# Kernel optimization log

Hardware: AMD Instinct MI355X
Metric: run time of the kernel (lower is better)

Reference implementation:

```python
import jax, jax.numpy as jnp
import numpy as np

B, S, D = 1, 2048, 2048
H, KVH = 32, 8
HD = D // H          # 64
N_REP = H // KVH     # 4
ROPE_THETA = 10000.0
NEG = -1e9


def setup_inputs() -> dict:
    key = jax.random.key(0)
    ks = jax.random.split(key, 8)
    x = jax.random.normal(ks[0], (B, S, D), dtype=jnp.float32)
    # RoPE tables: freqs_cis[t, j] = exp(i * t * theta^{-2j/HD}), j in [0, HD/2)
    inv_freq = 1.0 / (ROPE_THETA ** (jnp.arange(0, HD, 2, dtype=jnp.float32) / HD))
    angles = jnp.arange(S, dtype=jnp.float32)[:, None] * inv_freq[None, :]  # (S, HD/2)
    freqs_cos = jnp.cos(angles)
    freqs_sin = jnp.sin(angles)
    # causal additive mask (S, S)
    mask = jnp.where(jnp.tril(jnp.ones((S, S), dtype=bool)), 0.0, NEG).astype(jnp.float32)
    sc = 0.02
    wq = jax.random.normal(ks[1], (D, H * HD), dtype=jnp.float32) * sc
    wk = jax.random.normal(ks[2], (D, KVH * HD), dtype=jnp.float32) * sc
    wv = jax.random.normal(ks[3], (D, KVH * HD), dtype=jnp.float32) * sc
    wo = jax.random.normal(ks[4], (H * HD, D), dtype=jnp.float32) * sc
    fw = jax.random.normal(ks[5], (HD, HD), dtype=jnp.float32) * sc
    fb = jnp.zeros((HD,), dtype=jnp.float32)
    return {"x": x, "freqs_cos": freqs_cos, "freqs_sin": freqs_sin, "mask": mask,
            "wq": wq, "wk": wk, "wv": wv, "wo": wo, "fw": fw, "fb": fb,
            "start_pos": 0}


def _rope(t, cos, sin):
    # t: (B, S, h, HD) -> complex rotate pairs along last dim
    tr = t.reshape(*t.shape[:-1], HD // 2, 2)
    c = cos[None, :, None, :]  # (1, S, 1, HD/2)
    s = sin[None, :, None, :]
    re = tr[..., 0] * c - tr[..., 1] * s
    im = tr[..., 0] * s + tr[..., 1] * c
    return jnp.stack([re, im], axis=-1).reshape(t.shape)


def reference(x, freqs_cos, freqs_sin, mask, wq, wk, wv, wo, fw, fb, start_pos):
    b, s, _ = x.shape
    xq = (x @ wq).reshape(b, s, H, HD)
    xk = (x @ wk).reshape(b, s, KVH, HD)
    xv = (x @ wv).reshape(b, s, KVH, HD)
    xq = _rope(xq, freqs_cos, freqs_sin)
    xk = _rope(xk, freqs_cos, freqs_sin)
    # GQA: repeat kv heads (repeat_interleave on head dim)
    keys = jnp.repeat(xk, N_REP, axis=2)    # (b, s, H, HD)
    values = jnp.repeat(xv, N_REP, axis=2)
    q = xq.transpose(0, 2, 1, 3)            # (b, H, s, HD)
    k = keys.transpose(0, 2, 1, 3)
    v = values.transpose(0, 2, 1, 3)
    scores = jnp.einsum("bhqd,bhkd->bhqk", q, k) / np.sqrt(HD).astype(np.float32)
    scores = scores + mask[None, None, :, :]
    probs = jax.nn.softmax(scores.astype(jnp.float32), axis=-1).astype(q.dtype)
    out = jnp.einsum("bhqk,bhkd->bhqd", probs, v)  # (b, H, s, HD)
    # shared per-head FFN: Linear(HD, HD) + SiLU, vectorized over heads
    out = jax.nn.silu(out @ fw + fb)
    out = out.transpose(0, 2, 1, 3).reshape(b, s, H * HD)
    return out @ wo
```

## Files before the change

### kernel.cpp

```cpp
#include <hip/hip_runtime.h>
#include <stdint.h>

#define S_LEN 2048
#define DMODEL 2048
#define NH 32
#define NKV 8
#define HD 64

typedef __attribute__((ext_vector_type(8))) __bf16 bf16x8;
typedef __attribute__((ext_vector_type(4))) float f32x4;

__device__ __forceinline__ unsigned short f2bf(float f) {
    union { float f; uint32_t u; } v; v.f = f;
    uint32_t u = v.u;
    u += 0x7FFFu + ((u >> 16) & 1u);
    return (unsigned short)(u >> 16);
}

__device__ __forceinline__ uint32_t cvt_pk_bf16(float lo, float hi) {
    uint32_t r;
    asm("v_cvt_pk_bf16_f32 %0, %1, %2" : "=v"(r) : "v"(lo), "v"(hi));
    return r;
}

#define GLDS16(g, l)                                                          \
    __builtin_amdgcn_global_load_lds(                                         \
        (const __attribute__((address_space(1))) unsigned int*)(g),           \
        (__attribute__((address_space(3))) unsigned int*)(l), 16, 0, 0)

__global__ void cast_bf16_kernel(const float* __restrict__ src,
                                 unsigned short* __restrict__ dst, int n) {
    int g = (blockIdx.x * blockDim.x + threadIdx.x) * 8;
    if (g >= n) return;
    float4 a = *(const float4*)&src[g];
    float4 b = *(const float4*)&src[g + 4];
    unsigned short o[8];
    o[0] = f2bf(a.x); o[1] = f2bf(a.y); o[2] = f2bf(a.z); o[3] = f2bf(a.w);
    o[4] = f2bf(b.x); o[5] = f2bf(b.y); o[6] = f2bf(b.z); o[7] = f2bf(b.w);
    *(uint4*)&dst[g] = *(const uint4*)o;
}

__global__ void transpose_cast_kernel(const float* __restrict__ src,
                                      unsigned short* __restrict__ dst,
                                      int R, int C) {
    __shared__ float tile[32][33];
    int c0 = blockIdx.x * 32, r0 = blockIdx.y * 32;
    int tx = threadIdx.x, ty = threadIdx.y;
#pragma unroll
    for (int i = 0; i < 32; i += 8)
        tile[ty + i][tx] = src[(size_t)(r0 + ty + i) * C + c0 + tx];
    __syncthreads();
#pragma unroll
    for (int i = 0; i < 32; i += 8)
        dst[(size_t)(c0 + ty + i) * R + r0 + tx] = f2bf(tile[tx][ty + i]);
}

__global__ __launch_bounds__(256) void gemm_bt_kernel(
    const unsigned short* __restrict__ A, const unsigned short* __restrict__ BT,
    float* __restrict__ C0, float* __restrict__ C1, int M, int N,
    int Kstride, int Klen) {
    __shared__ unsigned short As[2][128 * 32];
    __shared__ unsigned short Bs[2][128 * 32];
    const int t = threadIdx.x;
    const int lane = t & 63, wave = t >> 6;
    const int wr = wave >> 1, wc = wave & 1;
    const int m0 = blockIdx.x * 128, n0 = blockIdx.y * 128;
    const int koff = blockIdx.z * Klen;
    float* __restrict__ C = blockIdx.z ? C1 : C0;
    const int l15 = lane & 15, lhi = lane >> 4;
    f32x4 acc[4][4] = {};
    const unsigned short* ga = A + (size_t)(m0 + (t >> 2)) * Kstride + koff + (t & 3) * 8;
    const unsigned short* gb = BT + (size_t)(n0 + (t >> 2)) * Kstride + koff + (t & 3) * 8;

    GLDS16(ga, &As[0][t * 8]);
    GLDS16(ga + (size_t)64 * Kstride, &As[0][t * 8 + 64 * 32]);
    GLDS16(gb, &Bs[0][t * 8]);
    GLDS16(gb + (size_t)64 * Kstride, &Bs[0][t * 8 + 64 * 32]);
    __syncthreads();

    int cur = 0;
    for (int k0 = 0; k0 < Klen; k0 += 32) {
        if (k0 + 32 < Klen) {
            GLDS16(ga + k0 + 32, &As[cur ^ 1][t * 8]);
            GLDS16(ga + (size_t)64 * Kstride + k0 + 32, &As[cur ^ 1][t * 8 + 64 * 32]);
            GLDS16(gb + k0 + 32, &Bs[cur ^ 1][t * 8]);
            GLDS16(gb + (size_t)64 * Kstride + k0 + 32, &Bs[cur ^ 1][t * 8 + 64 * 32]);
        }
        bf16x8 af[4], bfr[4];
#pragma unroll
        for (int m = 0; m < 4; m++)
            af[m] = *(const bf16x8*)&As[cur][(wr * 64 + m * 16 + l15) * 32 + lhi * 8];
#pragma unroll
        for (int n = 0; n < 4; n++)
            bfr[n] = *(const bf16x8*)&Bs[cur][(wc * 64 + n * 16 + l15) * 32 + lhi * 8];
#pragma unroll
        for (int m = 0; m < 4; m++)
#pragma unroll
            for (int n = 0; n < 4; n++)
                acc[m][n] = __builtin_amdgcn_mfma_f32_16x16x32_bf16(
                    af[m], bfr[n], acc[m][n], 0, 0, 0);
        __syncthreads();
        cur ^= 1;
    }
#pragma unroll
    for (int m = 0; m < 4; m++) {
        int row = m0 + wr * 64 + m * 16 + lhi * 4;
#pragma unroll
        for (int n = 0; n < 4; n++) {
            int col = n0 + wc * 64 + n * 16 + l15;
#pragma unroll
            for (int r = 0; r < 4; r++)
                C[(size_t)(row + r) * N + col] = acc[m][n][r];
        }
    }
}

__global__ void add_f32_kernel(float* __restrict__ out,
                               const float* __restrict__ p1, int n4) {
    int g = blockIdx.x * blockDim.x + threadIdx.x;
    if (g >= n4) return;
    float4 a = *(const float4*)&out[g * 4];
    float4 b = *(const float4*)&p1[g * 4];
    a.x += b.x; a.y += b.y; a.z += b.z; a.w += b.w;
    *(float4*)&out[g * 4] = a;
}

__global__ void rope_q_kernel(const float* __restrict__ Cqkv,
                              const float* __restrict__ cb,
                              const float* __restrict__ sb,
                              unsigned short* __restrict__ Q) {
    const float CS = 0.125f * 1.44269504f;
    int g = blockIdx.x * 256 + threadIdx.x;
    int i = g & 31;
    int h = (g >> 5) & 31;
    int s = g >> 10;
    float2 v = *(const float2*)&Cqkv[(size_t)s * 3072 + h * 64 + 2 * i];
    float cc = cb[s * 32 + i], ss = sb[s * 32 + i];
    ushort2 o;
    o.x = f2bf((v.x * cc - v.y * ss) * CS);
    o.y = f2bf((v.x * ss + v.y * cc) * CS);
    *(ushort2*)&Q[(size_t)h * (S_LEN * HD) + s * HD + 2 * i] = o;
}

__global__ void rope_k_kernel(const float* __restrict__ Cqkv,
                              const float* __restrict__ cb,
                              const float* __restrict__ sb,
                              unsigned short* __restrict__ Kb) {
    int g = blockIdx.x * 256 + threadIdx.x;
    int i = g & 31;
    int kvh = (g >> 5) & 7;
    int s = g >> 8;
    float2 v = *(const float2*)&Cqkv[(size_t)s * 3072 + 2048 + kvh * 64 + 2 * i];
    float cc = cb[s * 32 + i], ss = sb[s * 32 + i];
    ushort2 o;
    o.x = f2bf(v.x * cc - v.y * ss);
    o.y = f2bf(v.x * ss + v.y * cc);
    *(ushort2*)&Kb[(size_t)kvh * (S_LEN * HD) + s * HD + 2 * i] = o;
}

__global__ void v_transpose_kernel(const float* __restrict__ Cqkv,
                                   unsigned short* __restrict__ VT) {
    __shared__ float tile[32][33];
    int kvh = blockIdx.z;
    int d0 = blockIdx.x * 32, s0 = blockIdx.y * 32;
    int tx = threadIdx.x, ty = threadIdx.y;
#pragma unroll
    for (int i = 0; i < 32; i += 8)
        tile[ty + i][tx] =
            Cqkv[(size_t)(s0 + ty + i) * 3072 + 2560 + kvh * 64 + d0 + tx];
    __syncthreads();
#pragma unroll
    for (int i = 0; i < 32; i += 8)
        VT[(size_t)kvh * (HD * S_LEN) + (size_t)(d0 + ty + i) * S_LEN + s0 + tx] =
            f2bf(tile[tx][ty + i]);
}

__global__ __launch_bounds__(256) void flash_kernel(
    const unsigned short* __restrict__ Q, const unsigned short* __restrict__ Kg,
    const unsigned short* __restrict__ VTg, unsigned short* __restrict__ O) {
    __shared__ unsigned short Ks[2][4096];
    __shared__ unsigned short Vs[2][4096];
    const int t = threadIdx.x, lane = t & 63, wave = t >> 6;
    const int l15 = lane & 15, lhi = lane >> 4;
    const int bid = blockIdx.x;
    const int h = bid & 31;
    const int u = bid >> 5;
    const int grp = u >> 3, pos = u & 7;
    const int qt = (grp & 1) ? (grp * 8 + 7 - pos) : (grp * 8 + pos);
    const int kvh = h >> 2;

    const int srow = t >> 3;
    const int scol = ((t & 7) * 8) ^ ((srow & 7) * 8);
    const unsigned short* gk = Kg + ((size_t)kvh * S_LEN + srow) * HD + scol;
    const unsigned short* gv = VTg + ((size_t)kvh * HD + srow) * S_LEN + scol;

    const int q0 = qt * 64;
    const int nt = qt + 1;
    const int wq = q0 + wave * 16;
    const int q = wq + l15;

    const unsigned short* qp = Q + ((size_t)h * S_LEN + q) * HD + lhi * 8;
    bf16x8 qf0 = *(const bf16x8*)qp;
    bf16x8 qf1 = *(const bf16x8*)(qp + 32);

    f32x4 oacc[4] = {};
    float mrun = -1e30f, lrun = 0.f;

    GLDS16(gk, &Ks[0][t * 8]);
    GLDS16(gk + (size_t)32 * HD, &Ks[0][t * 8 + 2048]);
    GLDS16(gv, &Vs[0][t * 8]);
    GLDS16(gv + (size_t)32 * S_LEN, &Vs[0][t * 8 + 2048]);
    __syncthreads();

    int cur = 0;
#pragma unroll 1
    for (int kt = 0; kt < nt; ++kt) {
        const int kv0 = kt * 64;
        if (kt + 1 < nt) {
            GLDS16(gk + (size_t)(kv0 + 64) * HD, &Ks[cur ^ 1][t * 8]);
            GLDS16(gk + (size_t)(kv0 + 96) * HD, &Ks[cur ^ 1][t * 8 + 2048]);
            GLDS16(gv + (kv0 + 64), &Vs[cur ^ 1][t * 8]);
            GLDS16(gv + (size_t)32 * S_LEN + (kv0 + 64), &Vs[cur ^ 1][t * 8 + 2048]);
        }
        f32x4 sacc[4] = {};
#pragma unroll
        for (int nb = 0; nb < 4; nb++) {
            int krow = nb * 16 + l15;
            const unsigned short* kb = &Ks[cur][krow * 64];
            int sw = (krow & 7) * 8;
            bf16x8 k0v = *(const bf16x8*)&kb[(lhi * 8) ^ sw];
            bf16x8 k1v = *(const bf16x8*)&kb[(32 + lhi * 8) ^ sw];
            sacc[nb] = __builtin_amdgcn_mfma_f32_16x16x32_bf16(k0v, qf0, sacc[nb], 0, 0, 0);
            sacc[nb] = __builtin_amdgcn_mfma_f32_16x16x32_bf16(k1v, qf1, sacc[nb], 0, 0, 0);
        }
        float pv[4][4];
        float lm = -1e30f;
        if (kv0 + 63 <= wq) {
#pragma unroll
            for (int nb = 0; nb < 4; nb++)
#pragma unroll
                for (int r = 0; r < 4; r++) {
                    float sv = sacc[nb][r];
                    pv[nb][r] = sv;
                    lm = fmaxf(lm, sv);
                }
        } else {
#pragma unroll
            for (int nb = 0; nb < 4; nb++) {
                int kvb = kv0 + nb * 16 + lhi * 4;
#pragma unroll
                for (int r = 0; r < 4; r++) {
                    float sv = (kvb + r <= q) ? sacc[nb][r] : -1e30f;
                    pv[nb][r] = sv;
                    lm = fmaxf(lm, sv);
                }
            }
        }
        if (!__all(lm - mrun <= 8.f)) {
            float rm = fmaxf(lm, __shfl_xor(lm, 16));
            rm = fmaxf(rm, __shfl_xor(rm, 32));
            float mnew = fmaxf(mrun, rm);
            float sc = exp2f(mrun - mnew);
            mrun = mnew;
            lrun *= sc;
#pragma unroll
            for (int db = 0; db < 4; db++) oacc[db] *= sc;
        }
        float rs = 0.f;
#pragma unroll
        for (int nb = 0; nb < 4; nb++)
#pragma unroll
            for (int r = 0; r < 4; r++) {
                float e = exp2f(pv[nb][r] - mrun);
                pv[nb][r] = e;
                rs += e;
            }
        lrun += rs;
        uint32_t pka[4], pkb[4];
#pragma unroll
        for (int nb = 0; nb < 4; nb++) {
            pka[nb] = cvt_pk_bf16(pv[nb][0], pv[nb][1]);
            pkb[nb] = cvt_pk_bf16(pv[nb][2], pv[nb][3]);
        }
        const bool selB = ((lhi >> 1) & 1);
        const bool hiR = (lhi & 1);
        const bool sendA = ((lhi ^ (lhi >> 1)) & 1);
#pragma unroll
        for (int ks = 0; ks < 2; ks++) {
            uint32_t A0 = selB ? pka[2 * ks + 1] : pka[2 * ks];
            uint32_t A1 = selB ? pkb[2 * ks + 1] : pkb[2 * ks];
            uint32_t W0 = selB ? pka[2 * ks] : pka[2 * ks + 1];
            uint32_t W1 = selB ? pkb[2 * ks] : pkb[2 * ks + 1];
            uint32_t B0 = __shfl_xor((int)W0, 32);
            uint32_t B1 = __shfl_xor((int)W1, 32);
            uint32_t S0 = sendA ? A0 : B0, S1 = sendA ? A1 : B1;
            uint32_t R0 = __shfl_xor((int)S0, 16);
            uint32_t R1 = __shfl_xor((int)S1, 16);
            uint32_t F0 = hiR ? R0 : (selB ? B0 : A0);
            uint32_t F1 = hiR ? R1 : (selB ? B1 : A1);
            uint32_t F2 = hiR ? (selB ? A0 : B0) : R0;
            uint32_t F3 = hiR ? (selB ? A1 : B1) : R1;
            uint4 fu = {F0, F1, F2, F3};
            bf16x8 pfrag = *(const bf16x8*)&fu;
#pragma unroll
            for (int db = 0; db < 4; db++) {
                int vrow = db * 16 + l15;
                bf16x8 vf = *(const bf16x8*)&Vs[cur][vrow * 64 + ((ks * 32 + lhi * 8) ^ ((vrow & 7) * 8))];
                oacc[db] = __builtin_amdgcn_mfma_f32_16x16x32_bf16(vf, pfrag, oacc[db], 0, 0, 0);
            }
        }
        __syncthreads();
        cur ^= 1;
    }
    lrun += __shfl_xor(lrun, 16);
    lrun += __shfl_xor(lrun, 32);
    float rinv = 1.f / lrun;
#pragma unroll
    for (int db = 0; db < 4; db++) {
        uint32_t o0 = cvt_pk_bf16(oacc[db][0] * rinv, oacc[db][1] * rinv);
        uint32_t o1 = cvt_pk_bf16(oacc[db][2] * rinv, oacc[db][3] * rinv);
        uint2 ov = {o0, o1};
        *(uint2*)&O[((size_t)h * S_LEN + q) * HD + db * 16 + lhi * 4] = ov;
    }
}

__global__ __launch_bounds__(256) void fw_silu_kernel(
    const unsigned short* __restrict__ AT, const unsigned short* __restrict__ fwT,
    const float* __restrict__ fb, unsigned short* __restrict__ h2) {
    const int t = threadIdx.x, lane = t & 63, wave = t >> 6;
    const int l15 = lane & 15, lhi = lane >> 4;
    const int r0 = blockIdx.x * 64 + wave * 16;
    const unsigned short* ap = AT + (size_t)(r0 + l15) * HD + lhi * 8;
    bf16x8 a0 = *(const bf16x8*)ap;
    bf16x8 a1 = *(const bf16x8*)(ap + 32);
    f32x4 acc[4] = {};
#pragma unroll
    for (int nb = 0; nb < 4; nb++) {
        const unsigned short* bp = fwT + (size_t)(nb * 16 + l15) * HD + lhi * 8;
        bf16x8 b0 = *(const bf16x8*)bp;
        bf16x8 b1 = *(const bf16x8*)(bp + 32);
        acc[nb] = __builtin_amdgcn_mfma_f32_16x16x32_bf16(a0, b0, acc[nb], 0, 0, 0);
        acc[nb] = __builtin_amdgcn_mfma_f32_16x16x32_bf16(a1, b1, acc[nb], 0, 0, 0);
    }
#pragma unroll
    for (int nb = 0; nb < 4; nb++) {
        int col = nb * 16 + l15;
        float bias = fb[col];
#pragma unroll
        for (int r = 0; r < 4; r++) {
            int row = r0 + lhi * 4 + r;
            int s = row & (S_LEN - 1), hh = row >> 11;
            float x = acc[nb][r] + bias;
            float sg = 1.f / (1.f + exp2f(-x * 1.44269504f));
            h2[(size_t)s * DMODEL + hh * HD + col] = f2bf(x * sg);
        }
    }
}

extern "C" void kernel_launch(void* const* d_in, const int* in_sizes, int n_in,
                              void* d_out, int out_size, void* d_ws, size_t ws_size,
                              hipStream_t stream) {
    const float* x = (const float*)d_in[0];
    const float* fcos = (const float*)d_in[1];
    const float* fsin = (const float*)d_in[2];
    const float* wq = (const float*)d_in[4];
    const float* wk = (const float*)d_in[5];
    const float* wv = (const float*)d_in[6];
    const float* wo = (const float*)d_in[7];
    const float* fw = (const float*)d_in[8];
    const float* fb = (const float*)d_in[9];
    float* out = (float*)d_out;

    char* ws = (char*)d_ws;
    size_t off = 0;
    auto alloc = [&](size_t bytes) {
        void* p = ws + off;
        off += (bytes + 255) & ~(size_t)255;
        return p;
    };
    unsigned short* wqkvT = (unsigned short*)alloc((size_t)3072 * 2048 * 2);
    unsigned short* woT   = (unsigned short*)alloc((size_t)2048 * 2048 * 2);
    unsigned short* fwT   = (unsigned short*)alloc((size_t)64 * 64 * 2);
    float*          Cqkv  = (float*)alloc((size_t)2048 * 3072 * 4);
    unsigned short* Qb    = (unsigned short*)alloc((size_t)NH * S_LEN * HD * 2);
    unsigned short* Kb    = (unsigned short*)alloc((size_t)NKV * S_LEN * HD * 2);
    unsigned short* VT    = (unsigned short*)alloc((size_t)NKV * HD * S_LEN * 2);
    unsigned short* xb    = (unsigned short*)alloc((size_t)2048 * 2048 * 2);
    unsigned short* attn = (unsigned short*)Cqkv;
    float* P1 = (float*)((char*)Cqkv + (size_t)NH * S_LEN * HD * 2);
    unsigned short* h2 = xb;

    dim3 tb(32, 8);
    cast_bf16_kernel<<<2048, 256, 0, stream>>>(x, xb, 2048 * 2048);
    transpose_cast_kernel<<<dim3(64, 64), tb, 0, stream>>>(wq, wqkvT, 2048, 2048);
    transpose_cast_kernel<<<dim3(16, 64), tb, 0, stream>>>(wk, wqkvT + (size_t)2048 * 2048, 2048, 512);
    transpose_cast_kernel<<<dim3(16, 64), tb, 0, stream>>>(wv, wqkvT + (size_t)2560 * 2048, 2048, 512);
    transpose_cast_kernel<<<dim3(64, 64), tb, 0, stream>>>(wo, woT, 2048, 2048);
    transpose_cast_kernel<<<dim3(2, 2), tb, 0, stream>>>(fw, fwT, 64, 64);

    gemm_bt_kernel<<<dim3(16, 24, 1), 256, 0, stream>>>(xb, wqkvT, Cqkv, nullptr,
                                                        2048, 3072, 2048, 2048);

    rope_q_kernel<<<8192, 256, 0, stream>>>(Cqkv, fcos, fsin, Qb);
    rope_k_kernel<<<2048, 256, 0, stream>>>(Cqkv, fcos, fsin, Kb);
    v_transpose_kernel<<<dim3(2, 64, 8), tb, 0, stream>>>(Cqkv, VT);

    flash_kernel<<<1024, 256, 0, stream>>>(Qb, Kb, VT, attn);

    fw_silu_kernel<<<1024, 256, 0, stream>>>(attn, fwT, fb, h2);

    gemm_bt_kernel<<<dim3(16, 16, 2), 256, 0, stream>>>(h2, woT, out, P1,
                                                        2048, 2048, 2048, 1024);
    add_f32_kernel<<<4096, 256, 0, stream>>>(out, P1, 1048576);
}
```

Baseline: 187.9 us.

## Rework flash attention with 32x32 MFMA, 128-row Q tiles, paired causal work and triple buffering

The flash attention kernel now gives each wave 32 query rows and uses 32x32x16 MFMA instructions, so each block covers 128 queries. Each block handles two paired Q tiles (s and 15-s) to balance causal work, and the grid shrinks to 256 blocks. K/V staging moves to a three-buffer ring with explicit vmcnt waits, so loads run two tiles ahead. The goals are better MFMA efficiency, fewer P shuffles and less load latency. The cost is fewer blocks than CUs (lower occupancy), and waves past the causal limit sit idle.

```diff
diff --git a/kernel.cpp b/kernel.cpp
--- a/kernel.cpp
+++ b/kernel.cpp
@@ -9,6 +9,7 @@
 
 typedef __attribute__((ext_vector_type(8))) __bf16 bf16x8;
 typedef __attribute__((ext_vector_type(4))) float f32x4;
+typedef __attribute__((ext_vector_type(16))) float f32x16;
 
 __device__ __forceinline__ unsigned short f2bf(float f) {
     union { float f; uint32_t u; } v; v.f = f;
@@ -178,15 +179,12 @@
 __global__ __launch_bounds__(256) void flash_kernel(
     const unsigned short* __restrict__ Q, const unsigned short* __restrict__ Kg,
     const unsigned short* __restrict__ VTg, unsigned short* __restrict__ O) {
-    __shared__ unsigned short Ks[2][4096];
-    __shared__ unsigned short Vs[2][4096];
+    __shared__ unsigned short Ks[3][4096];
+    __shared__ unsigned short Vs[3][4096];
     const int t = threadIdx.x, lane = t & 63, wave = t >> 6;
-    const int l15 = lane & 15, lhi = lane >> 4;
+    const int l31 = lane & 31, hi = lane >> 5;
     const int bid = blockIdx.x;
-    const int h = bid & 31;
-    const int u = bid >> 5;
-    const int grp = u >> 3, pos = u & 7;
-    const int qt = (grp & 1) ? (grp * 8 + 7 - pos) : (grp * 8 + pos);
+    const int h = bid & 31, pr = bid >> 5;
     const int kvh = h >> 2;
 
     const int srow = t >> 3;
@@ -194,133 +192,153 @@
     const unsigned short* gk = Kg + ((size_t)kvh * S_LEN + srow) * HD + scol;
     const unsigned short* gv = VTg + ((size_t)kvh * HD + srow) * S_LEN + scol;
 
-    const int q0 = qt * 64;
-    const int nt = qt + 1;
-    const int wq = q0 + wave * 16;
-    const int q = wq + l15;
-
-    const unsigned short* qp = Q + ((size_t)h * S_LEN + q) * HD + lhi * 8;
-    bf16x8 qf0 = *(const bf16x8*)qp;
-    bf16x8 qf1 = *(const bf16x8*)(qp + 32);
-
-    f32x4 oacc[4] = {};
-    float mrun = -1e30f, lrun = 0.f;
-
-    GLDS16(gk, &Ks[0][t * 8]);
-    GLDS16(gk + (size_t)32 * HD, &Ks[0][t * 8 + 2048]);
-    GLDS16(gv, &Vs[0][t * 8]);
-    GLDS16(gv + (size_t)32 * S_LEN, &Vs[0][t * 8 + 2048]);
-    __syncthreads();
-
-    int cur = 0;
 #pragma unroll 1
-    for (int kt = 0; kt < nt; ++kt) {
-        const int kv0 = kt * 64;
-        if (kt + 1 < nt) {
-            GLDS16(gk + (size_t)(kv0 + 64) * HD, &Ks[cur ^ 1][t * 8]);
-            GLDS16(gk + (size_t)(kv0 + 96) * HD, &Ks[cur ^ 1][t * 8 + 2048]);
-            GLDS16(gv + (kv0 + 64), &Vs[cur ^ 1][t * 8]);
-            GLDS16(gv + (size_t)32 * S_LEN + (kv0 + 64), &Vs[cur ^ 1][t * 8 + 2048]);
+    for (int item = 0; item < 2; ++item) {
+        const int s = item ? (15 - pr) : pr;
+        const int q0 = s * 128;
+        const int nt = 2 * s + 2;
+        const int qw0 = q0 + wave * 32;
+        const int q = qw0 + l31;
+
+        const unsigned short* qp = Q + ((size_t)h * S_LEN + q) * HD + hi * 8;
+        bf16x8 qf0 = *(const bf16x8*)(qp);
+        bf16x8 qf1 = *(const bf16x8*)(qp + 16);
+        bf16x8 qf2 = *(const bf16x8*)(qp + 32);
+        bf16x8 qf3 = *(const bf16x8*)(qp + 48);
+
+        f32x16 oacc0 = {}, oacc1 = {};
+        float mrun = -1e30f, lrun = 0.f;
+
+        asm volatile("s_waitcnt vmcnt(0)" ::: "memory");
+        __builtin_amdgcn_s_barrier();
+        GLDS16(gk, &Ks[0][t * 8]);
+        GLDS16(gk + (size_t)32 * HD, &Ks[0][t * 8 + 2048]);
+        GLDS16(gv, &Vs[0][t * 8]);
+        GLDS16(gv + (size_t)32 * S_LEN, &Vs[0][t * 8 + 2048]);
+        GLDS16(gk + (size_t)64 * HD, &Ks[1][t * 8]);
+        GLDS16(gk + (size_t)96 * HD, &Ks[1][t * 8 + 2048]);
+        GLDS16(gv + 64, &Vs[1][t * 8]);
+        GLDS16(gv + (size_t)32 * S_LEN + 64, &Vs[1][t * 8 + 2048]);
+
+#pragma unroll 1
+        for (int kt = 0; kt < nt; ++kt) {
+            if (kt + 1 < nt) asm volatile("s_waitcnt vmcnt(4)" ::: "memory");
+            else             asm volatile("s_waitcnt vmcnt(0)" ::: "memory");
+            __builtin_amdgcn_s_barrier();
+            __builtin_amdgcn_sched_barrier(0);
+            if (kt + 2 < nt) {
+                const int pb = (kt + 2) % 3;
+                const size_t kvp = (size_t)(kt + 2) * 64;
+                GLDS16(gk + kvp * HD, &Ks[pb][t * 8]);
+                GLDS16(gk + (kvp + 32) * HD, &Ks[pb][t * 8 + 2048]);
+                GLDS16(gv + kvp, &Vs[pb][t * 8]);
+                GLDS16(gv + (size_t)32 * S_LEN + kvp, &Vs[pb][t * 8 + 2048]);
+            }
+            const int kv0 = kt * 64;
+            if (kv0 > qw0 + 31) continue;
+            const int cb = kt % 3;
+            const unsigned short* ksb = Ks[cb];
+            const unsigned short* vsb = Vs[cb];
+            const int sw = (l31 & 7) * 8;
+            f32x16 s0 = {}, s1 = {};
+#pragma unroll
+            for (int kc = 0; kc < 4; kc++) {
+                bf16x8 k0 = *(const bf16x8*)&ksb[l31 * 64 + ((16 * kc + 8 * hi) ^ sw)];
+                bf16x8 k1 = *(const bf16x8*)&ksb[(32 + l31) * 64 + ((16 * kc + 8 * hi) ^ sw)];
+                bf16x8 qc = (kc == 0) ? qf0 : (kc == 1) ? qf1 : (kc == 2) ? qf2 : qf3;
+                s0 = __builtin_amdgcn_mfma_f32_32x32x16_bf16(k0, qc, s0, 0, 0, 0);
+                s1 = __builtin_amdgcn_mfma_f32_32x32x16_bf16(k1, qc, s1, 0, 0, 0);
+            }
+            float p0[16], p1[16];
+            if (kv0 + 63 <= qw0) {
+#pragma unroll
+                for (int r = 0; r < 16; r++) { p0[r] = s0[r]; p1[r] = s1[r]; }
+            } else {
+#pragma unroll
+                for (int r = 0; r < 16; r++) {
+                    int rr = (r & 3) + 8 * (r >> 2) + 4 * hi;
+                    p0[r] = (kv0 + rr <= q) ? s0[r] : -1e30f;
+                    p1[r] = (kv0 + 32 + rr <= q) ? s1[r] : -1e30f;
+                }
+            }
+            float t8[8];
+#pragma unroll
+            for (int r = 0; r < 8; r++)
+                t8[r] = fmaxf(fmaxf(p0[r], p0[r + 8]), fmaxf(p1[r], p1[r + 8]));
+            float lm = fmaxf(fmaxf(fmaxf(t8[0], t8[4]), fmaxf(t8[1], t8[5])),
+                             fmaxf(fmaxf(t8[2], t8[6]), fmaxf(t8[3], t8[7])));
+            if (!__all(lm - mrun <= 8.f)) {
+                float rm = fmaxf(lm, __shfl_xor(lm, 32));
+                float mnew = fmaxf(mrun, rm);
+                float sc = exp2f(mrun - mnew);
+                mrun = mnew;
+                lrun *= sc;
+                oacc0 *= sc;
+                oacc1 *= sc;
+            }
+#pragma unroll
+            for (int r = 0; r < 16; r++) {
+                p0[r] = exp2f(p0[r] - mrun);
+                p1[r] = exp2f(p1[r] - mrun);
+            }
+            float sA = 0.f, sB = 0.f, sC = 0.f, sD = 0.f;
+#pragma unroll
+            for (int r = 0; r < 4; r++) {
+                sA += p0[r] + p1[r];
+                sB += p0[r + 4] + p1[r + 4];
+                sC += p0[r + 8] + p1[r + 8];
+                sD += p0[r + 12] + p1[r + 12];
+            }
+            lrun += (sA + sB) + (sC + sD);
+            bf16x8 pf[4];
+#pragma unroll
+            for (int kc = 0; kc < 4; kc++) {
+                const int sub = (kc & 1) * 8;
+                uint32_t Wl0, Wl1, Wh0, Wh1;
+                if (kc < 2) {
+                    Wl0 = cvt_pk_bf16(p0[sub + 0], p0[sub + 1]);
+                    Wl1 = cvt_pk_bf16(p0[sub + 2], p0[sub + 3]);
+                    Wh0 = cvt_pk_bf16(p0[sub + 4], p0[sub + 5]);
+                    Wh1 = cvt_pk_bf16(p0[sub + 6], p0[sub + 7]);
+                } else {
+                    Wl0 = cvt_pk_bf16(p1[sub + 0], p1[sub + 1]);
+                    Wl1 = cvt_pk_bf16(p1[sub + 2], p1[sub + 3]);
+                    Wh0 = cvt_pk_bf16(p1[sub + 4], p1[sub + 5]);
+                    Wh1 = cvt_pk_bf16(p1[sub + 6], p1[sub + 7]);
+                }
+                uint32_t sw0 = hi ? Wl0 : Wh0, sw1 = hi ? Wl1 : Wh1;
+                uint32_t rc0 = __shfl_xor((int)sw0, 32);
+                uint32_t rc1 = __shfl_xor((int)sw1, 32);
+                uint32_t kp0 = hi ? Wh0 : Wl0, kp1 = hi ? Wh1 : Wl1;
+                uint32_t F0 = hi ? rc0 : kp0;
+                uint32_t F1 = hi ? rc1 : kp1;
+                uint32_t F2 = hi ? kp0 : rc0;
+                uint32_t F3 = hi ? kp1 : rc1;
+                uint4 fu = {F0, F1, F2, F3};
+                pf[kc] = *(const bf16x8*)&fu;
+            }
+#pragma unroll
+            for (int kc = 0; kc < 4; kc++) {
+                bf16x8 v0 = *(const bf16x8*)&vsb[l31 * 64 + ((16 * kc + 8 * hi) ^ sw)];
+                bf16x8 v1 = *(const bf16x8*)&vsb[(32 + l31) * 64 + ((16 * kc + 8 * hi) ^ sw)];
+                oacc0 = __builtin_amdgcn_mfma_f32_32x32x16_bf16(v0, pf[kc], oacc0, 0, 0, 0);
+                oacc1 = __builtin_amdgcn_mfma_f32_32x32x16_bf16(v1, pf[kc], oacc1, 0, 0, 0);
+            }
         }
-        f32x4 sacc[4] = {};
-#pragma unroll
-        for (int nb = 0; nb < 4; nb++) {
-            int krow = nb * 16 + l15;
-            const unsigned short* kb = &Ks[cur][krow * 64];
-            int sw = (krow & 7) * 8;
-            bf16x8 k0v = *(const bf16x8*)&kb[(lhi * 8) ^ sw];
-            bf16x8 k1v = *(const bf16x8*)&kb[(32 + lhi * 8) ^ sw];
-            sacc[nb] = __builtin_amdgcn_mfma_f32_16x16x32_bf16(k0v, qf0, sacc[nb], 0, 0, 0);
-            sacc[nb] = __builtin_amdgcn_mfma_f32_16x16x32_bf16(k1v, qf1, sacc[nb], 0, 0, 0);
+        lrun += __shfl_xor(lrun, 32);
+        float rinv = 1.f / lrun;
+        unsigned short* ob = O + ((size_t)h * S_LEN + q) * HD + 4 * hi;
+#pragma unroll
+        for (int g = 0; g < 4; g++) {
+            uint32_t a0 = cvt_pk_bf16(oacc0[4 * g] * rinv, oacc0[4 * g + 1] * rinv);
+            uint32_t a1 = cvt_pk_bf16(oacc0[4 * g + 2] * rinv, oacc0[4 * g + 3] * rinv);
+            uint2 u0 = {a0, a1};
+            *(uint2*)(ob + 8 * g) = u0;
+            uint32_t b0 = cvt_pk_bf16(oacc1[4 * g] * rinv, oacc1[4 * g + 1] * rinv);
+            uint32_t b1 = cvt_pk_bf16(oacc1[4 * g + 2] * rinv, oacc1[4 * g + 3] * rinv);
+            uint2 u1 = {b0, b1};
+            *(uint2*)(ob + 32 + 8 * g) = u1;
         }
-        float pv[4][4];
-        float lm = -1e30f;
-        if (kv0 + 63 <= wq) {
-#pragma unroll
-            for (int nb = 0; nb < 4; nb++)
-#pragma unroll
-                for (int r = 0; r < 4; r++) {
-                    float sv = sacc[nb][r];
-                    pv[nb][r] = sv;
-                    lm = fmaxf(lm, sv);
-                }
-        } else {
-#pragma unroll
-            for (int nb = 0; nb < 4; nb++) {
-                int kvb = kv0 + nb * 16 + lhi * 4;
-#pragma unroll
-                for (int r = 0; r < 4; r++) {
-                    float sv = (kvb + r <= q) ? sacc[nb][r] : -1e30f;
-                    pv[nb][r] = sv;
-                    lm = fmaxf(lm, sv);
-                }
-            }
-        }
-        if (!__all(lm - mrun <= 8.f)) {
-            float rm = fmaxf(lm, __shfl_xor(lm, 16));
-            rm = fmaxf(rm, __shfl_xor(rm, 32));
-            float mnew = fmaxf(mrun, rm);
-            float sc = exp2f(mrun - mnew);
-            mrun = mnew;
-            lrun *= sc;
-#pragma unroll
-            for (int db = 0; db < 4; db++) oacc[db] *= sc;
-        }
-        float rs = 0.f;
-#pragma unroll
-        for (int nb = 0; nb < 4; nb++)
-#pragma unroll
-            for (int r = 0; r < 4; r++) {
-                float e = exp2f(pv[nb][r] - mrun);
-                pv[nb][r] = e;
-                rs += e;
-            }
-        lrun += rs;
-        uint32_t pka[4], pkb[4];
-#pragma unroll
-        for (int nb = 0; nb < 4; nb++) {
-            pka[nb] = cvt_pk_bf16(pv[nb][0], pv[nb][1]);
-            pkb[nb] = cvt_pk_bf16(pv[nb][2], pv[nb][3]);
-        }
-        const bool selB = ((lhi >> 1) & 1);
-        const bool hiR = (lhi & 1);
-        const bool sendA = ((lhi ^ (lhi >> 1)) & 1);
-#pragma unroll
-        for (int ks = 0; ks < 2; ks++) {
-            uint32_t A0 = selB ? pka[2 * ks + 1] : pka[2 * ks];
-            uint32_t A1 = selB ? pkb[2 * ks + 1] : pkb[2 * ks];
-            uint32_t W0 = selB ? pka[2 * ks] : pka[2 * ks + 1];
-            uint32_t W1 = selB ? pkb[2 * ks] : pkb[2 * ks + 1];
-            uint32_t B0 = __shfl_xor((int)W0, 32);
-            uint32_t B1 = __shfl_xor((int)W1, 32);
-            uint32_t S0 = sendA ? A0 : B0, S1 = sendA ? A1 : B1;
-            uint32_t R0 = __shfl_xor((int)S0, 16);
-            uint32_t R1 = __shfl_xor((int)S1, 16);
-            uint32_t F0 = hiR ? R0 : (selB ? B0 : A0);
-            uint32_t F1 = hiR ? R1 : (selB ? B1 : A1);
-            uint32_t F2 = hiR ? (selB ? A0 : B0) : R0;
-            uint32_t F3 = hiR ? (selB ? A1 : B1) : R1;
-            uint4 fu = {F0, F1, F2, F3};
-            bf16x8 pfrag = *(const bf16x8*)&fu;
-#pragma unroll
-            for (int db = 0; db < 4; db++) {
-                int vrow = db * 16 + l15;
-                bf16x8 vf = *(const bf16x8*)&Vs[cur][vrow * 64 + ((ks * 32 + lhi * 8) ^ ((vrow & 7) * 8))];
-                oacc[db] = __builtin_amdgcn_mfma_f32_16x16x32_bf16(vf, pfrag, oacc[db], 0, 0, 0);
-            }
-        }
-        __syncthreads();
-        cur ^= 1;
-    }
-    lrun += __shfl_xor(lrun, 16);
-    lrun += __shfl_xor(lrun, 32);
-    float rinv = 1.f / lrun;
-#pragma unroll
-    for (int db = 0; db < 4; db++) {
-        uint32_t o0 = cvt_pk_bf16(oacc[db][0] * rinv, oacc[db][1] * rinv);
-        uint32_t o1 = cvt_pk_bf16(oacc[db][2] * rinv, oacc[db][3] * rinv);
-        uint2 ov = {o0, o1};
-        *(uint2*)&O[((size_t)h * S_LEN + q) * HD + db * 16 + lhi * 4] = ov;
     }
 }
 
@@ -405,7 +423,7 @@
     rope_k_kernel<<<2048, 256, 0, stream>>>(Cqkv, fcos, fsin, Kb);
     v_transpose_kernel<<<dim3(2, 64, 8), tb, 0, stream>>>(Cqkv, VT);
 
-    flash_kernel<<<1024, 256, 0, stream>>>(Qb, Kb, VT, attn);
+    flash_kernel<<<256, 256, 0, stream>>>(Qb, Kb, VT, attn);
 
     fw_silu_kernel<<<1024, 256, 0, stream>>>(attn, fwT, fb, h2);
 
```

Result: slower. 194.9 us (+3.7%).
